# Performance work log

Measured on AMD Instinct MI355X. Metric: run time of the kernel, lower is better.

## Reference

```python
import jax, jax.numpy as jnp
import numpy as np

B, N, C = 2, 4096, 1024
HEADS = 16
BUCKET = 64
N_HASHES = 4
DH = C // HEADS
TOKEN_SELF_ATTN_VALUE = -5e4  # self-attention strongly discouraged (shared QK)


def setup_inputs() -> dict:
    key = jax.random.key(0)
    ks = jax.random.split(key, 8)
    s = 0.02
    n_buckets = N // BUCKET
    return {
        "queries": jax.random.normal(ks[0], (B, N, C), jnp.float32),
        "keys": jax.random.normal(ks[1], (B, N, C), jnp.float32),
        "values": jax.random.normal(ks[2], (B, N, C), jnp.float32),
        "attn_mask": jnp.zeros((1,), jnp.float32),
        "Wqk": jax.random.normal(ks[3], (C, C), jnp.float32) * s,
        "Wv": jax.random.normal(ks[4], (C, C), jnp.float32) * s,
        "Wout": jax.random.normal(ks[5], (C, C), jnp.float32) * s,
        "bout": jnp.zeros((C,), jnp.float32),
        # LSH random rotations, shared across batch and heads (reformer_pytorch default)
        "rotations": jax.random.normal(ks[6], (DH, N_HASHES, n_buckets // 2), jnp.float32),
        "tau": 1,
        "delta": 1,
    }


def _look_one_back(x):
    # concat each chunk with the previous chunk (wrap-around), along the kv axis
    extra = jnp.concatenate([x[:, -1:], x[:, :-1]], axis=1)
    return jnp.concatenate([x, extra], axis=2)


def _lsh_attention(qk, v, rotations, bucket_size, n_hashes):
    # qk, v: (bh, t, d); rotations: (d, n_hashes, n_buckets//2)
    bh, t, d = qk.shape
    n_buckets = t // bucket_size

    # --- hash vectors into buckets ---
    rotated = jnp.einsum('btf,fhi->bhti', qk, rotations)
    rotated = jnp.concatenate([rotated, -rotated], axis=-1)      # (bh, H, t, n_buckets)
    buckets = jnp.argmax(rotated, axis=-1)                       # (bh, H, t)
    offsets = (jnp.arange(n_hashes) * n_buckets)[None, :, None]
    buckets = (buckets + offsets).reshape(bh, n_hashes * t)

    # --- stable sort tokens by (bucket, position) ---
    ticker = jnp.arange(n_hashes * t)
    buckets_and_t = t * buckets + (ticker % t)[None, :]
    sticker = jnp.argsort(buckets_and_t, axis=-1)                # stable
    undo_sort = jnp.argsort(sticker, axis=-1)
    st = sticker % t                                             # original token idx per slot

    sqk = jnp.take_along_axis(qk, st[:, :, None], axis=1)
    sv = jnp.take_along_axis(v, st[:, :, None], axis=1)

    # --- chunk into n_hashes*n_buckets chunks of bucket_size ---
    n_chunks = n_hashes * n_buckets
    bq_t = st.reshape(bh, n_chunks, bucket_size)
    bqk = sqk.reshape(bh, n_chunks, bucket_size, d)
    bv = sv.reshape(bh, n_chunks, bucket_size, d)

    bq = bqk
    norm = jnp.linalg.norm(bqk, axis=-1, keepdims=True)
    bk = bqk / jnp.maximum(norm, 1e-12)                          # F.normalize, shared QK

    bk = _look_one_back(bk)
    bv = _look_one_back(bv)
    bkv_t = _look_one_back(bq_t)

    dots = jnp.einsum('bcie,bcje->bcij', bq, bk) * (d ** -0.5)   # (bh, nc, bs, 2*bs)
    self_mask = bq_t[..., :, None] == bkv_t[..., None, :]
    dots = jnp.where(self_mask, TOKEN_SELF_ATTN_VALUE, dots)

    dots_lse = jax.nn.logsumexp(dots, axis=-1, keepdims=True)
    probs = jnp.exp(dots - dots_lse)
    bo = jnp.einsum('bcij,bcje->bcie', probs, bv)

    # --- unsort and combine hash rounds by softmax over per-round logsumexps ---
    so = bo.reshape(bh, n_hashes * t, d)
    slogits = dots_lse.reshape(bh, n_hashes * t)
    o = jnp.take_along_axis(so, undo_sort[:, :, None], axis=1)
    logits = jnp.take_along_axis(slogits, undo_sort, axis=1)
    o = o.reshape(bh, n_hashes, t, d)
    logits = logits.reshape(bh, n_hashes, t, 1)
    w = jnp.exp(logits - jax.nn.logsumexp(logits, axis=1, keepdims=True))
    return jnp.sum(o * w, axis=1)                                # (bh, t, d)


def _forward(queries, Wqk, Wv, Wout, bout, rotations):
    b, n, c = queries.shape
    pad = (-n) % (BUCKET * 2)
    x = jnp.pad(queries, ((0, 0), (0, pad), (0, 0))) if pad else queries
    t = x.shape[1]
    qk = x @ Wqk.T
    v = x @ Wv.T
    qkh = qk.reshape(b, t, HEADS, DH).transpose(0, 2, 1, 3).reshape(b * HEADS, t, DH)
    vh = v.reshape(b, t, HEADS, DH).transpose(0, 2, 1, 3).reshape(b * HEADS, t, DH)
    oh = _lsh_attention(qkh, vh, rotations, BUCKET, N_HASHES)
    o = oh.reshape(b, HEADS, t, DH).transpose(0, 2, 1, 3).reshape(b, t, c)
    out = o @ Wout.T + bout
    return out[:, :n, :]


def reference(queries, keys, values, attn_mask, Wqk, Wv, Wout, bout, rotations, tau, delta):
    # keys/values/attn_mask/tau/delta are accepted but unused, as in the original layer
    return _forward(queries, Wqk, Wv, Wout, bout, rotations)
```

## Files before the change

### kernel.cpp

```cpp
#include <hip/hip_runtime.h>
#include <hip/hip_bf16.h>
#include <math.h>


#define SG_COMPUTE(BUF)                                                      \
    {                                                                        \
        _Pragma("unroll")                                                    \
        for (int kk = 0; kk < 8; ++kk) {                                     \
            float a[8], b[8];                                                \
            *(float4*)&a[0] = *(const float4*)&As[BUF][kk][tx * 8];          \
            *(float4*)&a[4] = *(const float4*)&As[BUF][kk][tx * 8 + 4];      \
            *(float4*)&b[0] = *(const float4*)&Bs[BUF][kk][ty * 8];          \
            *(float4*)&b[4] = *(const float4*)&Bs[BUF][kk][ty * 8 + 4];      \
            _Pragma("unroll")                                                \
            for (int i = 0; i < 8; ++i)                                      \
                _Pragma("unroll")                                            \
                for (int j = 0; j < 8; ++j)                                  \
                    acc[i][j] = fmaf(a[i], b[j], acc[i][j]);                 \
        }                                                                    \
    }

__global__ __launch_bounds__(256) void sgemm128(const float* __restrict__ A,
                                                const float* __restrict__ W,
                                                float* __restrict__ out,
                                                int headLayout,
                                                const float* __restrict__ bias) {
    __shared__ float As[2][8][128];
    __shared__ float Bs[2][8][128];
    int tid = threadIdx.x;
    int tx = tid & 15, ty = tid >> 4;
    int id = blockIdx.x;
    int swz = (id & 7) * 64 + (id >> 3);
    int m0 = (swz & 63) * 128;
    int n0 = (swz >> 6) * 128;
    int lr = tid >> 1;
    int lk = (tid & 1) * 4;
    const float* pA = &A[(size_t)(m0 + lr) * 1024 + lk];
    const float* pB = &W[(size_t)(n0 + lr) * 1024 + lk];
    float acc[8][8];
#pragma unroll
    for (int i = 0; i < 8; ++i)
#pragma unroll
        for (int j = 0; j < 8; ++j) acc[i][j] = 0.f;

    float4 av = *(const float4*)&pA[0];
    float4 bv = *(const float4*)&pB[0];
    As[0][lk + 0][lr] = av.x; As[0][lk + 1][lr] = av.y;
    As[0][lk + 2][lr] = av.z; As[0][lk + 3][lr] = av.w;
    Bs[0][lk + 0][lr] = bv.x; Bs[0][lk + 1][lr] = bv.y;
    Bs[0][lk + 2][lr] = bv.z; Bs[0][lk + 3][lr] = bv.w;
    __syncthreads();

    for (int it = 0; it < 127; ++it) {
        int cur = it & 1;
        int nxt = cur ^ 1;
        av = *(const float4*)&pA[(it + 1) * 8];
        bv = *(const float4*)&pB[(it + 1) * 8];
        SG_COMPUTE(cur)
        As[nxt][lk + 0][lr] = av.x; As[nxt][lk + 1][lr] = av.y;
        As[nxt][lk + 2][lr] = av.z; As[nxt][lk + 3][lr] = av.w;
        Bs[nxt][lk + 0][lr] = bv.x; Bs[nxt][lk + 1][lr] = bv.y;
        Bs[nxt][lk + 2][lr] = bv.z; Bs[nxt][lk + 3][lr] = bv.w;
        __syncthreads();
    }
    SG_COMPUTE(1)

#pragma unroll
    for (int i = 0; i < 8; ++i) {
        int m = m0 + tx * 8 + i;
        int bb = m >> 12, t = m & 4095;
#pragma unroll
        for (int j = 0; j < 8; ++j) {
            int n = n0 + ty * 8 + j;
            float val = acc[i][j];
            if (bias) val += bias[n];
            if (headLayout) {
                out[(((size_t)(bb * 16 + (n >> 6))) * 4096 + t) * 64 + (n & 63)] = val;
            } else {
                out[(size_t)m * 1024 + n] = val;
            }
        }
    }
}
#undef SG_COMPUTE

__global__ __launch_bounds__(256) void bucket32(const float* __restrict__ qk,
                                                const float* __restrict__ rot,
                                                int* __restrict__ keys) {
    int tid = threadIdx.x;
    int blk = blockIdx.x;
    int token = (blk & 15) * 256 + tid;
    int r = (blk >> 4) & 3;
    int bh = blk >> 6;
    const float* q = &qk[((size_t)bh * 4096 + token) * 64];
    float racc[32];
#pragma unroll
    for (int i = 0; i < 32; ++i) racc[i] = 0.f;
    for (int f0 = 0; f0 < 64; f0 += 4) {
        float4 qv = *(const float4*)&q[f0];
        const float* rp0 = &rot[(f0 + 0) * 128 + r * 32];
        const float* rp1 = rp0 + 128;
        const float* rp2 = rp0 + 256;
        const float* rp3 = rp0 + 384;
#pragma unroll
        for (int i = 0; i < 32; ++i) racc[i] = fmaf(qv.x, rp0[i], racc[i]);
#pragma unroll
        for (int i = 0; i < 32; ++i) racc[i] = fmaf(qv.y, rp1[i], racc[i]);
#pragma unroll
        for (int i = 0; i < 32; ++i) racc[i] = fmaf(qv.z, rp2[i], racc[i]);
#pragma unroll
        for (int i = 0; i < 32; ++i) racc[i] = fmaf(qv.w, rp3[i], racc[i]);
    }
    float best = -INFINITY;
    int bi = 0;
#pragma unroll
    for (int i = 0; i < 32; ++i) { if (racc[i] > best) { best = racc[i]; bi = i; } }
#pragma unroll
    for (int i = 0; i < 32; ++i) { float x = -racc[i]; if (x > best) { best = x; bi = 32 + i; } }
    int bin = r * 64 + bi;
    keys[(size_t)bh * 16384 + r * 4096 + token] = bin * 4096 + token;
}

#define PST 257

__global__ __launch_bounds__(256) void countsort_kernel(const int* __restrict__ keys,
                                                        int* __restrict__ st_sorted) {
    __shared__ unsigned short pre[64 * PST];
    __shared__ unsigned char sbin[4096];
    __shared__ unsigned short sperm[4096];
    __shared__ int qsum[64 * 4];
    __shared__ int qoff[64 * 4];
    __shared__ int binOffset[64];

    int tid = threadIdx.x;
    int bh = blockIdx.x >> 2;
    int r = blockIdx.x & 3;
    const int* kb = &keys[(((size_t)bh * 4 + r) << 12)];

    for (int u = tid; u < 64 * PST; u += 256) pre[u] = 0;
    __syncthreads();

    int base = tid << 4;
#pragma unroll
    for (int u = 0; u < 4; ++u) {
        int4 kv = *(const int4*)&kb[base + u * 4];
        int b0 = (kv.x >> 12) & 63;
        int b1 = (kv.y >> 12) & 63;
        int b2 = (kv.z >> 12) & 63;
        int b3 = (kv.w >> 12) & 63;
        sbin[base + u * 4 + 0] = (unsigned char)b0;
        sbin[base + u * 4 + 1] = (unsigned char)b1;
        sbin[base + u * 4 + 2] = (unsigned char)b2;
        sbin[base + u * 4 + 3] = (unsigned char)b3;
        pre[b0 * PST + tid]++;
        pre[b1 * PST + tid]++;
        pre[b2 * PST + tid]++;
        pre[b3 * PST + tid]++;
    }
    __syncthreads();

    int b = tid & 63, q = tid >> 6;
    {
        int run = 0;
        for (int i = 0; i < 64; ++i) run += pre[b * PST + q * 64 + i];
        qsum[b * 4 + q] = run;
    }
    __syncthreads();

    if (tid < 64) {
        int s0 = qsum[tid * 4 + 0], s1 = qsum[tid * 4 + 1];
        int s2 = qsum[tid * 4 + 2], s3 = qsum[tid * 4 + 3];
        qoff[tid * 4 + 0] = 0;
        qoff[tid * 4 + 1] = s0;
        qoff[tid * 4 + 2] = s0 + s1;
        qoff[tid * 4 + 3] = s0 + s1 + s2;
        binOffset[tid] = s0 + s1 + s2 + s3;
    }
    __syncthreads();
    if (tid == 0) {
        int running = 0;
        for (int i = 0; i < 64; ++i) {
            int t = binOffset[i];
            binOffset[i] = running;
            running += t;
        }
    }
    __syncthreads();

    {
        int run2 = qoff[b * 4 + q];
        for (int i = 0; i < 64; ++i) {
            int idx = b * PST + q * 64 + i;
            int t = pre[idx];
            pre[idx] = (unsigned short)run2;
            run2 += t;
        }
    }
    __syncthreads();

#pragma unroll
    for (int k = 0; k < 16; ++k) {
        int bin = sbin[base + k];
        int off = pre[bin * PST + tid]++;
        sperm[binOffset[bin] + off] = (unsigned short)(base + k);
    }
    __syncthreads();

    int* ob = &st_sorted[(((size_t)bh * 4 + r) << 12)];
#pragma unroll
    for (int u = 0; u < 16; ++u) ob[u * 256 + tid] = (int)sperm[u * 256 + tid];
}

__global__ __launch_bounds__(256) void attn_kernel(const float* __restrict__ qk,
                                                   const float* __restrict__ v,
                                                   const int* __restrict__ st_sorted,
                                                   float* __restrict__ o4,
                                                   float* __restrict__ lse4) {
    __shared__ float bufA[128 * 68];
    __shared__ float red[64 * 17];
    __shared__ int posl[128];
    __shared__ float invl[128];

    int tid = threadIdx.x;
    int bh = blockIdx.x >> 8;
    int c = blockIdx.x & 255;
    int r = c >> 6;
    int pc = (c + 255) & 255;
    const int* stb = &st_sorted[(size_t)bh * 16384];
    if (tid < 64) posl[tid] = stb[c * 64 + tid];
    else if (tid < 128) posl[tid] = stb[pc * 64 + (tid - 64)];
    __syncthreads();

    float* kqt = bufA;
    for (int u = 0; u < 8; ++u) {
        int flat = u * 256 + tid;
        int row = flat >> 4;
        int f4 = (flat & 15) * 4;
        size_t gbase = ((size_t)bh * 4096 + posl[row]) * 64 + f4;
        float4 qv = *(const float4*)&qk[gbase];
        int rw = row ^ ((((f4 >> 2)) & 7) << 2);
        kqt[(f4 + 0) * 132 + rw] = qv.x;
        kqt[(f4 + 1) * 132 + rw] = qv.y;
        kqt[(f4 + 2) * 132 + rw] = qv.z;
        kqt[(f4 + 3) * 132 + rw] = qv.w;
    }
    __syncthreads();

    if (tid < 128) {
        float ss = 0.f;
        for (int f = 0; f < 64; ++f) {
            int s = ((f >> 2) & 7) << 2;
            float x = kqt[f * 132 + (tid ^ s)];
            ss += x * x;
        }
        invl[tid] = 1.0f / fmaxf(sqrtf(ss), 1e-12f);
    }
    __syncthreads();

    int tx = tid & 15, ty = tid >> 4;
    float acc[4][8];
#pragma unroll
    for (int i = 0; i < 4; ++i)
#pragma unroll
        for (int j = 0; j < 8; ++j) acc[i][j] = 0.f;
    for (int f = 0; f < 64; ++f) {
        int s = ((f >> 2) & 7) << 2;
        float a[4], b[8];
        *(float4*)a = *(const float4*)&kqt[f * 132 + ((tx * 4) ^ s)];
        *(float4*)&b[0] = *(const float4*)&kqt[f * 132 + ((ty * 8) ^ s)];
        *(float4*)&b[4] = *(const float4*)&kqt[f * 132 + ((ty * 8 + 4) ^ s)];
#pragma unroll
        for (int i = 0; i < 4; ++i)
#pragma unroll
            for (int j = 0; j < 8; ++j) acc[i][j] = fmaf(a[i], b[j], acc[i][j]);
    }

    int qp[4];
#pragma unroll
    for (int ii = 0; ii < 4; ++ii) qp[ii] = posl[tx * 4 + ii];
#pragma unroll
    for (int jj = 0; jj < 8; ++jj) {
        int j = ty * 8 + jj;
        float sc = invl[j] * 0.125f;
        int kp = posl[j];
#pragma unroll
        for (int ii = 0; ii < 4; ++ii) {
            float x = acc[ii][jj] * sc;
            acc[ii][jj] = (qp[ii] == kp) ? -5e4f : x;
        }
    }

#pragma unroll
    for (int ii = 0; ii < 4; ++ii) {
        float pm = acc[ii][0];
#pragma unroll
        for (int jj = 1; jj < 8; ++jj) pm = fmaxf(pm, acc[ii][jj]);
        red[(tx * 4 + ii) * 17 + ty] = pm;
    }
    __syncthreads();
    float m[4];
#pragma unroll
    for (int ii = 0; ii < 4; ++ii) {
        float mm = red[(tx * 4 + ii) * 17 + 0];
        for (int t = 1; t < 16; ++t) mm = fmaxf(mm, red[(tx * 4 + ii) * 17 + t]);
        m[ii] = mm;
    }
    __syncthreads();

    float* pT = bufA;
    float ps[4] = {0.f, 0.f, 0.f, 0.f};
#pragma unroll
    for (int jj = 0; jj < 8; ++jj) {
        int j = ty * 8 + jj;
        float e0 = __expf(acc[0][jj] - m[0]);
        float e1 = __expf(acc[1][jj] - m[1]);
        float e2 = __expf(acc[2][jj] - m[2]);
        float e3 = __expf(acc[3][jj] - m[3]);
        ps[0] += e0; ps[1] += e1; ps[2] += e2; ps[3] += e3;
        float4 ev; ev.x = e0; ev.y = e1; ev.z = e2; ev.w = e3;
        *(float4*)&pT[j * 68 + tx * 4] = ev;
    }
#pragma unroll
    for (int ii = 0; ii < 4; ++ii) red[(tx * 4 + ii) * 17 + ty] = ps[ii];
    __syncthreads();
    float l[4];
#pragma unroll
    for (int ii = 0; ii < 4; ++ii) {
        float s = 0.f;
        for (int t = 0; t < 16; ++t) s += red[(tx * 4 + ii) * 17 + t];
        l[ii] = s;
    }

    if (ty == 0) {
#pragma unroll
        for (int ii = 0; ii < 4; ++ii) {
            int i = tx * 4 + ii;
            lse4[((size_t)bh * 4 + r) * 4096 + posl[i]] = m[ii] + __logf(l[ii]);
        }
    }

    const float* vb = v + (size_t)bh * 4096 * 64 + ty * 4;
    float acc2[4][4];
#pragma unroll
    for (int i = 0; i < 4; ++i)
#pragma unroll
        for (int j = 0; j < 4; ++j) acc2[i][j] = 0.f;

    float4 p0 = *(const float4*)&vb[(size_t)posl[0] * 64];
    float4 p1 = *(const float4*)&vb[(size_t)posl[1] * 64];
    float4 p2 = *(const float4*)&vb[(size_t)posl[2] * 64];
    float4 p3 = *(const float4*)&vb[(size_t)posl[3] * 64];
    for (int j0 = 0; j0 < 128; j0 += 4) {
        float4 c0 = p0, c1 = p1, c2 = p2, c3 = p3;
        if (j0 + 4 < 128) {
            p0 = *(const float4*)&vb[(size_t)posl[j0 + 4] * 64];
            p1 = *(const float4*)&vb[(size_t)posl[j0 + 5] * 64];
            p2 = *(const float4*)&vb[(size_t)posl[j0 + 6] * 64];
            p3 = *(const float4*)&vb[(size_t)posl[j0 + 7] * 64];
        }
#define PVSTEP(JJ, CV)                                                       \
        {                                                                    \
            float a_[4];                                                     \
            *(float4*)a_ = *(const float4*)&pT[(j0 + (JJ)) * 68 + tx * 4];   \
            acc2[0][0] = fmaf(a_[0], CV.x, acc2[0][0]);                      \
            acc2[0][1] = fmaf(a_[0], CV.y, acc2[0][1]);                      \
            acc2[0][2] = fmaf(a_[0], CV.z, acc2[0][2]);                      \
            acc2[0][3] = fmaf(a_[0], CV.w, acc2[0][3]);                      \
            acc2[1][0] = fmaf(a_[1], CV.x, acc2[1][0]);                      \
            acc2[1][1] = fmaf(a_[1], CV.y, acc2[1][1]);                      \
            acc2[1][2] = fmaf(a_[1], CV.z, acc2[1][2]);                      \
            acc2[1][3] = fmaf(a_[1], CV.w, acc2[1][3]);                      \
            acc2[2][0] = fmaf(a_[2], CV.x, acc2[2][0]);                      \
            acc2[2][1] = fmaf(a_[2], CV.y, acc2[2][1]);                      \
            acc2[2][2] = fmaf(a_[2], CV.z, acc2[2][2]);                      \
            acc2[2][3] = fmaf(a_[2], CV.w, acc2[2][3]);                      \
            acc2[3][0] = fmaf(a_[3], CV.x, acc2[3][0]);                      \
            acc2[3][1] = fmaf(a_[3], CV.y, acc2[3][1]);                      \
            acc2[3][2] = fmaf(a_[3], CV.z, acc2[3][2]);                      \
            acc2[3][3] = fmaf(a_[3], CV.w, acc2[3][3]);                      \
        }
        PVSTEP(0, c0)
        PVSTEP(1, c1)
        PVSTEP(2, c2)
        PVSTEP(3, c3)
#undef PVSTEP
    }
#pragma unroll
    for (int ii = 0; ii < 4; ++ii) {
        int i = tx * 4 + ii;
        float rl = 1.0f / l[ii];
        size_t ob = (((size_t)bh * 4 + r) * 4096 + posl[i]) * 64 + ty * 4;
        float4 ov;
        ov.x = acc2[ii][0] * rl;
        ov.y = acc2[ii][1] * rl;
        ov.z = acc2[ii][2] * rl;
        ov.w = acc2[ii][3] * rl;
        *(float4*)&o4[ob] = ov;
    }
}

__global__ __launch_bounds__(256) void combine_kernel(const float* __restrict__ o4,
                                                      const float* __restrict__ lse4,
                                                      float* __restrict__ o_bt) {
    int tid = threadIdx.x;
    int gt = blockIdx.x * 4 + (tid >> 6);
    int d = tid & 63;
    int bh = gt >> 12, p = gt & 4095;
    size_t base = ((size_t)bh * 4) * 4096 + p;
    float l0 = lse4[base];
    float l1 = lse4[base + 4096];
    float l2 = lse4[base + 8192];
    float l3 = lse4[base + 12288];
    float mm = fmaxf(fmaxf(l0, l1), fmaxf(l2, l3));
    float w0 = __expf(l0 - mm), w1 = __expf(l1 - mm);
    float w2 = __expf(l2 - mm), w3 = __expf(l3 - mm);
    float W = w0 + w1 + w2 + w3;
    size_t ob = (((size_t)bh * 4) * 4096 + p) * 64 + d;
    const size_t rs = (size_t)4096 * 64;
    float o = w0 * o4[ob]
            + w1 * o4[ob + rs]
            + w2 * o4[ob + 2 * rs]
            + w3 * o4[ob + 3 * rs];
    int b = bh >> 4, h = bh & 15;
    o_bt[((size_t)b * 4096 + p) * 1024 + h * 64 + d] = o / W;
}

extern "C" void kernel_launch(void* const* d_in, const int* in_sizes, int n_in,
                              void* d_out, int out_size, void* d_ws, size_t ws_size,
                              hipStream_t stream) {
    const float* x    = (const float*)d_in[0];
    const float* Wqk  = (const float*)d_in[4];
    const float* Wv   = (const float*)d_in[5];
    const float* Wout = (const float*)d_in[6];
    const float* bout = (const float*)d_in[7];
    const float* rot  = (const float*)d_in[8];
    float* out = (float*)d_out;

    char* ws = (char*)d_ws;
    float* qk32          = (float*)(ws);
    float* v             = (float*)(ws + 33554432);
    float* o4            = (float*)(ws + 67108864);
    float* lse4          = (float*)(ws + 201326592);
    int* keys            = (int*)(ws + 203423744);
    int* st_sorted       = (int*)(ws + 205520896);
    float* o_bt          = qk32;

    sgemm128<<<512, 256, 0, stream>>>(x, Wqk, qk32, 1, nullptr);
    sgemm128<<<512, 256, 0, stream>>>(x, Wv, v, 1, nullptr);
    bucket32<<<2048, 256, 0, stream>>>(qk32, rot, keys);
    countsort_kernel<<<128, 256, 0, stream>>>(keys, st_sorted);
    attn_kernel<<<8192, 256, 0, stream>>>(qk32, v, st_sorted, o4, lse4);
    combine_kernel<<<32768, 256, 0, stream>>>(o4, lse4, o_bt);
    sgemm128<<<512, 256, 0, stream>>>(o_bt, Wout, out, 0, bout);
}
```

Before: 1.165 ms.

## Shrink SGEMM tile to 128x64 with vectorized stores; precompute V byte offsets

The fp32 GEMM changes from 128x128 to 128x64 output tiles. That doubles the grid to 1024 blocks and lets each thread's 4 output columns be written as float4, contiguous within a head row. Only half the threads load B tiles, so per-thread accumulators drop from 64 to 32 and occupancy may rise, at the cost of lower arithmetic intensity per block. In the attention kernel, V gather offsets are precomputed as byte offsets in shared memory and a few loops are fully unrolled to cut address arithmetic.

Result: slower. 1.213 ms (+4.1%).

```diff
diff --git a/kernel.cpp b/kernel.cpp
--- a/kernel.cpp
+++ b/kernel.cpp
@@ -7,78 +7,87 @@
     {                                                                        \
         _Pragma("unroll")                                                    \
         for (int kk = 0; kk < 8; ++kk) {                                     \
-            float a[8], b[8];                                                \
-            *(float4*)&a[0] = *(const float4*)&As[BUF][kk][tx * 8];          \
-            *(float4*)&a[4] = *(const float4*)&As[BUF][kk][tx * 8 + 4];      \
-            *(float4*)&b[0] = *(const float4*)&Bs[BUF][kk][ty * 8];          \
-            *(float4*)&b[4] = *(const float4*)&Bs[BUF][kk][ty * 8 + 4];      \
+            float a[8], b[4];                                                \
+            *(float4*)&a[0] = *(const float4*)&As[BUF][kk][tx * 4];          \
+            *(float4*)&a[4] = *(const float4*)&As[BUF][kk][64 + tx * 4];     \
+            *(float4*)&b[0] = *(const float4*)&Bs[BUF][kk][ty * 4];          \
             _Pragma("unroll")                                                \
             for (int i = 0; i < 8; ++i)                                      \
                 _Pragma("unroll")                                            \
-                for (int j = 0; j < 8; ++j)                                  \
+                for (int j = 0; j < 4; ++j)                                  \
                     acc[i][j] = fmaf(a[i], b[j], acc[i][j]);                 \
         }                                                                    \
     }
 
-__global__ __launch_bounds__(256) void sgemm128(const float* __restrict__ A,
-                                                const float* __restrict__ W,
-                                                float* __restrict__ out,
-                                                int headLayout,
-                                                const float* __restrict__ bias) {
+__global__ __launch_bounds__(256) void sgemm64(const float* __restrict__ A,
+                                               const float* __restrict__ W,
+                                               float* __restrict__ out,
+                                               int headLayout,
+                                               const float* __restrict__ bias) {
     __shared__ float As[2][8][128];
-    __shared__ float Bs[2][8][128];
+    __shared__ float Bs[2][8][64];
     int tid = threadIdx.x;
     int tx = tid & 15, ty = tid >> 4;
     int id = blockIdx.x;
-    int swz = (id & 7) * 64 + (id >> 3);
-    int m0 = (swz & 63) * 128;
-    int n0 = (swz >> 6) * 128;
+    int swz = (id & 7) * 128 + (id >> 3);
+    int tm = swz & 63;
+    int tn = swz >> 6;
+    int m0 = tm * 128, n0 = tn * 64;
     int lr = tid >> 1;
     int lk = (tid & 1) * 4;
     const float* pA = &A[(size_t)(m0 + lr) * 1024 + lk];
-    const float* pB = &W[(size_t)(n0 + lr) * 1024 + lk];
-    float acc[8][8];
+    bool doB = (tid < 128);
+    int lrB = (tid & 127) >> 1;
+    const float* pB = &W[(size_t)(n0 + lrB) * 1024 + lk];
+    float acc[8][4];
 #pragma unroll
     for (int i = 0; i < 8; ++i)
 #pragma unroll
-        for (int j = 0; j < 8; ++j) acc[i][j] = 0.f;
+        for (int j = 0; j < 4; ++j) acc[i][j] = 0.f;
 
     float4 av = *(const float4*)&pA[0];
-    float4 bv = *(const float4*)&pB[0];
+    float4 bv;
+    if (doB) bv = *(const float4*)&pB[0];
     As[0][lk + 0][lr] = av.x; As[0][lk + 1][lr] = av.y;
     As[0][lk + 2][lr] = av.z; As[0][lk + 3][lr] = av.w;
-    Bs[0][lk + 0][lr] = bv.x; Bs[0][lk + 1][lr] = bv.y;
-    Bs[0][lk + 2][lr] = bv.z; Bs[0][lk + 3][lr] = bv.w;
+    if (doB) {
+        Bs[0][lk + 0][lrB] = bv.x; Bs[0][lk + 1][lrB] = bv.y;
+        Bs[0][lk + 2][lrB] = bv.z; Bs[0][lk + 3][lrB] = bv.w;
+    }
     __syncthreads();
 
     for (int it = 0; it < 127; ++it) {
         int cur = it & 1;
         int nxt = cur ^ 1;
         av = *(const float4*)&pA[(it + 1) * 8];
-        bv = *(const float4*)&pB[(it + 1) * 8];
+        if (doB) bv = *(const float4*)&pB[(it + 1) * 8];
         SG_COMPUTE(cur)
         As[nxt][lk + 0][lr] = av.x; As[nxt][lk + 1][lr] = av.y;
         As[nxt][lk + 2][lr] = av.z; As[nxt][lk + 3][lr] = av.w;
-        Bs[nxt][lk + 0][lr] = bv.x; Bs[nxt][lk + 1][lr] = bv.y;
-        Bs[nxt][lk + 2][lr] = bv.z; Bs[nxt][lk + 3][lr] = bv.w;
+        if (doB) {
+            Bs[nxt][lk + 0][lrB] = bv.x; Bs[nxt][lk + 1][lrB] = bv.y;
+            Bs[nxt][lk + 2][lrB] = bv.z; Bs[nxt][lk + 3][lrB] = bv.w;
+        }
         __syncthreads();
     }
     SG_COMPUTE(1)
 
+    float4 bias4 = make_float4(0.f, 0.f, 0.f, 0.f);
+    if (bias) bias4 = *(const float4*)&bias[n0 + ty * 4];
+    int h = n0 >> 6;
 #pragma unroll
     for (int i = 0; i < 8; ++i) {
-        int m = m0 + tx * 8 + i;
-        int bb = m >> 12, t = m & 4095;
-#pragma unroll
-        for (int j = 0; j < 8; ++j) {
-            int n = n0 + ty * 8 + j;
-            float val = acc[i][j];
-            if (bias) val += bias[n];
-            if (headLayout) {
-                out[(((size_t)(bb * 16 + (n >> 6))) * 4096 + t) * 64 + (n & 63)] = val;
-            } else {
-                out[(size_t)m * 1024 + n] = val;
-            }
+        int m = m0 + ((i < 4) ? (tx * 4 + i) : (64 + tx * 4 + (i - 4)));
+        float4 ov;
+        ov.x = acc[i][0] + bias4.x;
+        ov.y = acc[i][1] + bias4.y;
+        ov.z = acc[i][2] + bias4.z;
+        ov.w = acc[i][3] + bias4.w;
+        if (headLayout) {
+            int bb = m >> 12, t = m & 4095;
+            *(float4*)&out[(((size_t)(bb * 16 + h)) * 4096 + t) * 64 + ty * 4] = ov;
+        } else {
+            *(float4*)&out[(size_t)m * 1024 + n0 + ty * 4] = ov;
         }
     }
 }
@@ -219,6 +228,7 @@
     __shared__ float bufA[128 * 68];
     __shared__ float red[64 * 17];
     __shared__ int posl[128];
+    __shared__ int voff[128];
     __shared__ float invl[128];
 
     int tid = threadIdx.x;
@@ -227,11 +237,19 @@
     int r = c >> 6;
     int pc = (c + 255) & 255;
     const int* stb = &st_sorted[(size_t)bh * 16384];
-    if (tid < 64) posl[tid] = stb[c * 64 + tid];
-    else if (tid < 128) posl[tid] = stb[pc * 64 + (tid - 64)];
+    if (tid < 64) {
+        int p = stb[c * 64 + tid];
+        posl[tid] = p;
+        voff[tid] = p << 8;
+    } else if (tid < 128) {
+        int p = stb[pc * 64 + (tid - 64)];
+        posl[tid] = p;
+        voff[tid] = p << 8;
+    }
     __syncthreads();
 
     float* kqt = bufA;
+#pragma unroll
     for (int u = 0; u < 8; ++u) {
         int flat = u * 256 + tid;
         int row = flat >> 4;
@@ -263,6 +281,7 @@
     for (int i = 0; i < 4; ++i)
 #pragma unroll
         for (int j = 0; j < 8; ++j) acc[i][j] = 0.f;
+#pragma unroll
     for (int f = 0; f < 64; ++f) {
         int s = ((f >> 2) & 7) << 2;
         float a[4], b[8];
@@ -339,24 +358,25 @@
         }
     }
 
-    const float* vb = v + (size_t)bh * 4096 * 64 + ty * 4;
+    const char* vb8 = (const char*)v + ((size_t)bh << 20);
+    int coff = ty * 16;
     float acc2[4][4];
 #pragma unroll
     for (int i = 0; i < 4; ++i)
 #pragma unroll
         for (int j = 0; j < 4; ++j) acc2[i][j] = 0.f;
 
-    float4 p0 = *(const float4*)&vb[(size_t)posl[0] * 64];
-    float4 p1 = *(const float4*)&vb[(size_t)posl[1] * 64];
-    float4 p2 = *(const float4*)&vb[(size_t)posl[2] * 64];
-    float4 p3 = *(const float4*)&vb[(size_t)posl[3] * 64];
+    float4 p0 = *(const float4*)(vb8 + (voff[0] + coff));
+    float4 p1 = *(const float4*)(vb8 + (voff[1] + coff));
+    float4 p2 = *(const float4*)(vb8 + (voff[2] + coff));
+    float4 p3 = *(const float4*)(vb8 + (voff[3] + coff));
     for (int j0 = 0; j0 < 128; j0 += 4) {
         float4 c0 = p0, c1 = p1, c2 = p2, c3 = p3;
         if (j0 + 4 < 128) {
-            p0 = *(const float4*)&vb[(size_t)posl[j0 + 4] * 64];
-            p1 = *(const float4*)&vb[(size_t)posl[j0 + 5] * 64];
-            p2 = *(const float4*)&vb[(size_t)posl[j0 + 6] * 64];
-            p3 = *(const float4*)&vb[(size_t)posl[j0 + 7] * 64];
+            p0 = *(const float4*)(vb8 + (voff[j0 + 4] + coff));
+            p1 = *(const float4*)(vb8 + (voff[j0 + 5] + coff));
+            p2 = *(const float4*)(vb8 + (voff[j0 + 6] + coff));
+            p3 = *(const float4*)(vb8 + (voff[j0 + 7] + coff));
         }
 #define PVSTEP(JJ, CV)                                                       \
         {                                                                    \
@@ -445,11 +465,11 @@
     int* st_sorted       = (int*)(ws + 205520896);
     float* o_bt          = qk32;
 
-    sgemm128<<<512, 256, 0, stream>>>(x, Wqk, qk32, 1, nullptr);
-    sgemm128<<<512, 256, 0, stream>>>(x, Wv, v, 1, nullptr);
+    sgemm64<<<1024, 256, 0, stream>>>(x, Wqk, qk32, 1, nullptr);
+    sgemm64<<<1024, 256, 0, stream>>>(x, Wv, v, 1, nullptr);
     bucket32<<<2048, 256, 0, stream>>>(qk32, rot, keys);
     countsort_kernel<<<128, 256, 0, stream>>>(keys, st_sorted);
     attn_kernel<<<8192, 256, 0, stream>>>(qk32, v, st_sorted, o4, lse4);
     combine_kernel<<<32768, 256, 0, stream>>>(o4, lse4, o_bt);
-    sgemm128<<<512, 256, 0, stream>>>(o_bt, Wout, out, 0, bout);
-}
+    sgemm64<<<1024, 256, 0, stream>>>(o_bt, Wout, out, 0, bout);
+}
```
